# Kernel optimization log

Hardware: AMD Instinct MI355X
Metric: run time of the kernel (lower is better)

## Reference

```python
import jax, jax.numpy as jnp
import numpy as np

N, D, H, K = 131072, 512, 128, 3
NPOS, NNEG = 8192, 8192
KM_ITERS = 4
PROTO_SHIFT = 0.15
PROTO_LOGIT_SCALE = 0.2
TEMP = 2.5


def _sq_cdist(x, c):
    # squared euclidean distance, matches torch.cdist(...).pow(2)
    d = jnp.sum(x * x, -1, keepdims=True) + jnp.sum(c * c, -1)[None, :] - 2.0 * (x @ c.T)
    return jnp.maximum(d, 0.0)


def _kmeans(x, k, iters):
    # torch.linspace(0, n-1, steps=k).long() init, fixed iteration count
    n = x.shape[0]
    idx = jnp.linspace(0.0, n - 1, k).astype(jnp.int32)
    centers = x[idx]
    for _ in range(iters):
        assign = jnp.argmin(_sq_cdist(x, centers), axis=1)
        sums = jax.ops.segment_sum(x, assign, num_segments=k)
        counts = jax.ops.segment_sum(jnp.ones((n,), x.dtype), assign, num_segments=k)[:, None]
        # empty cluster keeps old center (mask.any() branch in torch)
        centers = jnp.where(counts > 0, sums / jnp.maximum(counts, 1.0), centers)
    return centers


def setup_inputs() -> dict:
    key = jax.random.key(0)
    ks = jax.random.split(key, 10)
    s = 1.0 / np.sqrt(D).astype(np.float32)
    return {
        "z_cls": jax.random.normal(ks[0], (N, D), jnp.float32),
        "z_proto": jax.random.normal(ks[1], (N, D), jnp.float32),
        "pos_ctx": jax.random.normal(ks[2], (D,), jnp.float32),
        "neg_ctx": jax.random.normal(ks[3], (D,), jnp.float32),
        "W1": jax.random.normal(ks[4], (H, D), jnp.float32) * s,
        "b1": jnp.zeros((H,), jnp.float32),
        "W2": jax.random.normal(ks[5], (1, H), jnp.float32) * (1.0 / np.sqrt(H).astype(np.float32)),
        "b2": jnp.zeros((1,), jnp.float32),
        "Wp": jax.random.normal(ks[6], (D, D), jnp.float32) * s,
        "bp": jnp.zeros((D,), jnp.float32),
        "Wn": jax.random.normal(ks[7], (D, D), jnp.float32) * s,
        "bn": jnp.zeros((D,), jnp.float32),
        "pos_idx": jax.random.randint(ks[8], (NPOS,), 0, N),
        "neg_idx": jax.random.randint(ks[9], (NNEG,), 0, N),
    }


def reference(z_cls, z_proto, pos_ctx, neg_ctx, W1, b1, W2, b2, Wp, bp, Wn, bn, pos_idx, neg_idx):
    # _build_prototypes (pos_idx/neg_idx nonempty path)
    pos_proto = _kmeans(z_proto[pos_idx], K, KM_ITERS)          # [K, D]
    neg_proto = jnp.mean(z_proto[neg_idx], axis=0)              # [D]
    # _calibrate (ema not initialized -> no EMA blend)
    pos_proto = pos_proto + PROTO_SHIFT * (pos_ctx @ Wp.T + bp)[None, :]
    neg_proto = neg_proto + PROTO_SHIFT * (neg_ctx @ Wn.T + bn)
    # distances
    d_pos_all = _sq_cdist(z_proto, pos_proto)                   # [N, K]
    d_pos = jnp.min(d_pos_all, axis=1)
    pos_assign = jnp.argmin(d_pos_all, axis=1)
    d_neg = jnp.mean((z_proto - neg_proto[None, :]) ** 2, axis=1)
    proto_logit = (d_neg - d_pos) / np.sqrt(D).astype(np.float32)
    # cls head (eval mode: dropout is identity)
    h = jax.nn.relu(z_cls @ W1.T + b1)
    cls_logit = (h @ W2.T + b2)[:, 0]
    logits = (cls_logit + PROTO_LOGIT_SCALE * proto_logit) / TEMP
    prob = jax.nn.sigmoid(logits)
    return (logits, prob, PROTO_LOGIT_SCALE * proto_logit, pos_assign, d_pos_all, pos_proto, neg_proto)
```

## Files before the change

### kernel.cpp

```cpp
#include <hip/hip_runtime.h>
#include <hip/hip_bf16.h>

#define NPTS 131072
#define DIM  512
#define HID  128
#define KCL  3
#define NPOSI 8192
#define NNEGI 8192

typedef __attribute__((ext_vector_type(8))) short bf16x8;
typedef __attribute__((ext_vector_type(4))) float f32x4;

#define ASG __attribute__((address_space(1)))
#define ASL __attribute__((address_space(3)))

enum {
  WS_SHIFT_POS = 0,
  WS_SHIFT_NEG = 512,
  WS_NEGSUM    = 1024,
  WS_NEGPART   = 1536,
  WS_SUMS      = 132608,
  WS_PPROTO    = 138764,
  WS_PN        = 140812,
  WS_W1FRAG    = 140816,
};
#define SUMS_STRIDE 1539

__device__ __forceinline__ short f2bf(float x) {
  __hip_bfloat16 h = __float2bfloat16(x);
  return *reinterpret_cast<short*>(&h);
}

__global__ __launch_bounds__(256, 1) void k_prep(const float* __restrict__ W1,
                                                 const float* __restrict__ Wp, const float* __restrict__ bp,
                                                 const float* __restrict__ Wn, const float* __restrict__ bn,
                                                 const float* __restrict__ pos_ctx, const float* __restrict__ neg_ctx,
                                                 const float* __restrict__ zp, const int* __restrict__ neg_idx,
                                                 float* __restrict__ ws) {
  int bid = blockIdx.x, t = threadIdx.x;
  if (bid < 32) {
    int fid = bid * 256 + t;
    int kc = fid >> 9;
    int n  = (fid >> 6) & 7;
    int l  = fid & 63;
    int row = n * 16 + (l & 15);
    int col = kc * 32 + (l >> 4) * 8;
    const float* src = W1 + (size_t)row * DIM + col;
    float4 v0 = *(const float4*)(src);
    float4 v1 = *(const float4*)(src + 4);
    bf16x8 f;
    f[0] = f2bf(v0.x); f[1] = f2bf(v0.y); f[2] = f2bf(v0.z); f[3] = f2bf(v0.w);
    f[4] = f2bf(v1.x); f[5] = f2bf(v1.y); f[6] = f2bf(v1.z); f[7] = f2bf(v1.w);
    ((bf16x8*)(ws + WS_W1FRAG))[fid] = f;
  } else if (bid < 64) {
    int b = bid - 32;
    int mat = b >> 4;
    const float* W    = mat ? Wn : Wp;
    const float* bias = mat ? bn : bp;
    const float* ctx  = mat ? neg_ctx : pos_ctx;
    float* outp = ws + (mat ? WS_SHIFT_NEG : WS_SHIFT_POS);
    int row = (b & 15) * 32 + (t >> 3);
    int sub = t & 7;
    const float* wr = W + row * DIM + sub * 64;
    const float* cr = ctx + sub * 64;
    float s = 0.f;
#pragma unroll
    for (int j = 0; j < 64; j += 4) {
      float4 w4 = *(const float4*)(wr + j);
      float4 c4 = *(const float4*)(cr + j);
      s += w4.x * c4.x + w4.y * c4.y + w4.z * c4.z + w4.w * c4.w;
    }
    s += __shfl_xor(s, 1);
    s += __shfl_xor(s, 2);
    s += __shfl_xor(s, 4);
    if (sub == 0) outp[row] = 0.15f * (s + bias[row]);
  } else if (bid < 320) {
    int jb = bid - 64;
    int c0 = t * 2;
    float a0 = 0.f, a1 = 0.f;
    int base = jb * 32;
#pragma unroll 8
    for (int jj = 0; jj < 32; ++jj) {
      int row = neg_idx[base + jj];
      float2 v = *(const float2*)(zp + (size_t)row * DIM + c0);
      a0 += v.x; a1 += v.y;
    }
    ws[WS_NEGPART + jb * DIM + c0]     = a0;
    ws[WS_NEGPART + jb * DIM + c0 + 1] = a1;
  } else {
    for (int idx = t; idx < 4 * SUMS_STRIDE; idx += 256) ws[WS_SUMS + idx] = 0.f;
  }
}

template <int IT>
__global__ __launch_bounds__(256) void k_km(const float* __restrict__ zp,
                                            const int* __restrict__ pos_idx,
                                            float* __restrict__ ws) {
  int bid = blockIdx.x, t = threadIdx.x;
  if (IT == 0 && bid == 256) {
    int c0 = t * 2;
    float a0 = 0.f, a1 = 0.f;
#pragma unroll 8
    for (int j = 0; j < 256; ++j) {
      float2 v = *(const float2*)(ws + WS_NEGPART + j * DIM + c0);
      a0 += v.x; a1 += v.y;
    }
    ws[WS_NEGSUM + c0]     = a0;
    ws[WS_NEGSUM + c0 + 1] = a1;
    return;
  }
  __shared__ float cc[KCL * DIM];
  __shared__ float cn[KCL];
  __shared__ float lsum[KCL * DIM];
  __shared__ float lcnt[KCL];
  int w = t >> 6, l = t & 63;

  for (int idx = t; idx < KCL * DIM; idx += 256) lsum[idx] = 0.f;
  if (t < KCL) lcnt[t] = 0.f;

  for (int idx = t; idx < KCL * DIM; idx += 256) {
    int k = idx >> 9;
    int sel = (k == 0) ? 0 : ((k == 1) ? 4095 : 8191);
    float v = zp[(size_t)pos_idx[sel] * DIM + (idx & 511)];
#pragma unroll
    for (int j = 0; j < IT; ++j) {
      float cntv = ws[WS_SUMS + j * SUMS_STRIDE + 3 * DIM + k];
      float sv   = ws[WS_SUMS + j * SUMS_STRIDE + idx];
      v = (cntv > 0.f) ? sv / cntv : v;
    }
    cc[idx] = v;
  }
  __syncthreads();
  if (w < KCL) {
    float s = 0.f;
#pragma unroll
    for (int m = 0; m < 8; ++m) { float v = cc[w * DIM + l + m * 64]; s += v * v; }
#pragma unroll
    for (int m = 1; m < 64; m <<= 1) s += __shfl_xor(s, m);
    if (l == 0) cn[w] = s;
  }
  __syncthreads();

  float ck0[8], ck1[8], ck2[8];
#pragma unroll
  for (int j = 0; j < 8; ++j) {
    ck0[j] = cc[0 * DIM + l * 8 + j];
    ck1[j] = cc[1 * DIM + l * 8 + j];
    ck2[j] = cc[2 * DIM + l * 8 + j];
  }
  float cn0 = cn[0], cn1 = cn[1], cn2 = cn[2];
  float acc0[8] = {0,0,0,0,0,0,0,0}, acc1[8] = {0,0,0,0,0,0,0,0}, acc2[8] = {0,0,0,0,0,0,0,0};
  float cnt0 = 0.f, cnt1 = 0.f, cnt2 = 0.f;

  int wid = bid * 4 + w;
#pragma unroll 2
  for (int p = wid; p < NPOSI; p += 1024) {
    int row = pos_idx[p];
    const float* xr = zp + (size_t)row * DIM + l * 8;
    float4 x0 = *(const float4*)(xr);
    float4 x1 = *(const float4*)(xr + 4);
    float x[8] = {x0.x, x0.y, x0.z, x0.w, x1.x, x1.y, x1.z, x1.w};
    float d0 = 0.f, d1 = 0.f, d2 = 0.f;
#pragma unroll
    for (int j = 0; j < 8; ++j) { d0 += x[j] * ck0[j]; d1 += x[j] * ck1[j]; d2 += x[j] * ck2[j]; }
#pragma unroll
    for (int m = 1; m < 64; m <<= 1) {
      d0 += __shfl_xor(d0, m); d1 += __shfl_xor(d1, m); d2 += __shfl_xor(d2, m);
    }
    float t0 = cn0 - 2.f * d0, t1 = cn1 - 2.f * d1, t2 = cn2 - 2.f * d2;
    int a = 0; float best = t0;
    if (t1 < best) { best = t1; a = 1; }
    if (t2 < best) { best = t2; a = 2; }
    if (a == 0)      { cnt0 += 1.f;
#pragma unroll
      for (int j = 0; j < 8; ++j) acc0[j] += x[j]; }
    else if (a == 1) { cnt1 += 1.f;
#pragma unroll
      for (int j = 0; j < 8; ++j) acc1[j] += x[j]; }
    else             { cnt2 += 1.f;
#pragma unroll
      for (int j = 0; j < 8; ++j) acc2[j] += x[j]; }
  }
#pragma unroll
  for (int j = 0; j < 8; ++j) {
    atomicAdd(&lsum[0 * DIM + l * 8 + j], acc0[j]);
    atomicAdd(&lsum[1 * DIM + l * 8 + j], acc1[j]);
    atomicAdd(&lsum[2 * DIM + l * 8 + j], acc2[j]);
  }
  if (l == 0) {
    atomicAdd(&lcnt[0], cnt0); atomicAdd(&lcnt[1], cnt1); atomicAdd(&lcnt[2], cnt2);
  }
  __syncthreads();
  for (int idx = t; idx < KCL * DIM; idx += 256) atomicAdd(&ws[WS_SUMS + IT * SUMS_STRIDE + idx], lsum[idx]);
  if (t < KCL) atomicAdd(&ws[WS_SUMS + IT * SUMS_STRIDE + 3 * DIM + t], lcnt[t]);
}

__global__ __launch_bounds__(256) void k_fin(const float* __restrict__ zp,
                                             const int* __restrict__ pos_idx,
                                             float* __restrict__ ws, float* __restrict__ out) {
  __shared__ __align__(16) float pp[4 * DIM];
  int t = threadIdx.x, w = t >> 6, l = t & 63;
  for (int idx = t; idx < KCL * DIM; idx += 256) {
    int k = idx >> 9, d = idx & 511;
    int sel = (k == 0) ? 0 : ((k == 1) ? 4095 : 8191);
    float v = zp[(size_t)pos_idx[sel] * DIM + d];
#pragma unroll
    for (int j = 0; j < 4; ++j) {
      float cntv = ws[WS_SUMS + j * SUMS_STRIDE + 3 * DIM + k];
      float sv   = ws[WS_SUMS + j * SUMS_STRIDE + idx];
      v = (cntv > 0.f) ? sv / cntv : v;
    }
    pp[idx] = v + ws[WS_SHIFT_POS + d];
  }
  for (int d = t; d < DIM; d += 256)
    pp[3 * DIM + d] = ws[WS_NEGSUM + d] * (1.f / NNEGI) + ws[WS_SHIFT_NEG + d];
  __syncthreads();
  {
    float s = 0.f;
#pragma unroll
    for (int m = 0; m < 8; ++m) { float v = pp[w * DIM + l + m * 64]; s += v * v; }
#pragma unroll
    for (int m = 1; m < 64; m <<= 1) s += __shfl_xor(s, m);
    if (l == 0) ws[WS_PN + w] = s;
  }
  for (int idx = t; idx < 4 * DIM; idx += 256) {
    ws[WS_PPROTO + idx] = pp[idx];
    out[7 * NPTS + idx] = pp[idx];
  }
}

__global__ __launch_bounds__(512) void k_fused(const float* __restrict__ zc,
                                               const float* __restrict__ zp,
                                               const float* __restrict__ b1,
                                               const float* __restrict__ W2,
                                               const float* __restrict__ b2,
                                               const float* __restrict__ ws,
                                               float* __restrict__ out) {
  __shared__ __align__(16) float Azc[16 * DIM];
  __shared__ __align__(16) float Azp[16 * DIM];
  __shared__ __align__(16) float pp[4 * DIM];
  __shared__ float pns[4];
  __shared__ float clsv[16];

  int t = threadIdx.x, w = t >> 6, l = t & 63;
  int bid = (blockIdx.x & 7) * 1024 + (blockIdx.x >> 3);
  int i0 = bid * 16;

  {
    int cg = (w < 4);
    int r0 = (cg ? w : (w - 4)) * 4;
    const float* gsrc = (cg ? zc : zp) + (size_t)(i0 + r0) * DIM;
    float* ldsb = cg ? Azc : Azp;
#pragma unroll
    for (int r = 0; r < 4; ++r) {
      int rloc = r0 + r;
      int swz = (rloc & 7) << 2;
#pragma unroll
      for (int seg = 0; seg < 2; ++seg) {
        int c = seg * 256 + ((l * 4) ^ swz);
        __builtin_amdgcn_global_load_lds((const ASG void*)(gsrc + (size_t)r * DIM + c),
                                         (ASL void*)&ldsb[rloc * DIM + seg * 256], 16, 0, 0);
      }
    }
  }

  if (t < 512) ((float4*)pp)[t] = ((const float4*)(ws + WS_PPROTO))[t];
  if (t < 16) clsv[t] = 0.f;
  if (t < 4) pns[t] = ws[WS_PN + t];
  int col_l = l & 15;
  float b1c[2], w2c[2], b2v = b2[0];
  if (w < 4) {
#pragma unroll
    for (int nn = 0; nn < 2; ++nn) {
      int col = (w * 2 + nn) * 16 + col_l;
      b1c[nn] = b1[col];
      w2c[nn] = W2[col];
    }
  }
  __syncthreads();

  float rd0 = 0.f, rd1 = 0.f, rd2 = 0.f, rdn = 0.f, rsx = 0.f;
  if (w < 4) {
    const bf16x8* w1f = (const bf16x8*)(ws + WS_W1FRAG);
    int sub = l >> 4, arow = l & 15;
    int swz = (arow & 7) << 2;
    int abase = arow * DIM;
    f32x4 acc[2];
    acc[0] = (f32x4){0.f, 0.f, 0.f, 0.f};
    acc[1] = (f32x4){0.f, 0.f, 0.f, 0.f};
    bf16x8 B2[3][2];
#pragma unroll
    for (int pf = 0; pf < 3; ++pf)
#pragma unroll
      for (int nn = 0; nn < 2; ++nn)
        B2[pf][nn] = w1f[pf * 512 + (w * 2 + nn) * 64 + l];

#pragma unroll
    for (int kc = 0; kc < 16; ++kc) {
      int g = kc * 32 + sub * 8;
      float4 a0 = *(const float4*)&Azc[abase + (g ^ swz)];
      float4 a1 = *(const float4*)&Azc[abase + ((g + 4) ^ swz)];
      if (kc + 3 < 16) {
#pragma unroll
        for (int nn = 0; nn < 2; ++nn)
          B2[kc % 3][nn] = w1f[(kc + 3) * 512 + (w * 2 + nn) * 64 + l];
      }
      bf16x8 af;
      af[0] = f2bf(a0.x); af[1] = f2bf(a0.y); af[2] = f2bf(a0.z); af[3] = f2bf(a0.w);
      af[4] = f2bf(a1.x); af[5] = f2bf(a1.y); af[6] = f2bf(a1.z); af[7] = f2bf(a1.w);
#pragma unroll
      for (int nn = 0; nn < 2; ++nn)
        acc[nn] = __builtin_amdgcn_mfma_f32_16x16x32_bf16(af, B2[kc % 3][nn], acc[nn], 0, 0, 0);
    }
    float prt[4] = {0.f, 0.f, 0.f, 0.f};
#pragma unroll
    for (int nn = 0; nn < 2; ++nn) {
#pragma unroll
      for (int r = 0; r < 4; ++r) {
        float h = acc[nn][r] + b1c[nn];
        h = h > 0.f ? h : 0.f;
        prt[r] += h * w2c[nn];
      }
    }
#pragma unroll
    for (int m = 1; m < 16; m <<= 1) {
#pragma unroll
      for (int r = 0; r < 4; ++r) prt[r] += __shfl_xor(prt[r], m);
    }
    if (col_l == 0) {
      float add = (w == 0) ? b2v : 0.f;
#pragma unroll
      for (int r = 0; r < 4; ++r)
        atomicAdd(&clsv[sub * 4 + r], prt[r] + add);
    }
  } else {
    int s = l & 15, r4 = l >> 4;
    int rloc = (w - 4) * 4 + r4;
    int swz = (rloc & 7) << 2;
    int xbase = rloc * DIM;
#pragma unroll
    for (int j = 0; j < 8; ++j) {
      int c = j * 64 + s * 4;
      float4 x  = *(const float4*)&Azp[xbase + (c ^ swz)];
      float4 c0 = *(const float4*)&pp[0 * DIM + c];
      float4 c1 = *(const float4*)&pp[1 * DIM + c];
      float4 c2 = *(const float4*)&pp[2 * DIM + c];
      float4 c3 = *(const float4*)&pp[3 * DIM + c];
      rd0 += x.x * c0.x + x.y * c0.y + x.z * c0.z + x.w * c0.w;
      rd1 += x.x * c1.x + x.y * c1.y + x.z * c1.z + x.w * c1.w;
      rd2 += x.x * c2.x + x.y * c2.y + x.z * c2.z + x.w * c2.w;
      rdn += x.x * c3.x + x.y * c3.y + x.z * c3.z + x.w * c3.w;
      rsx += x.x * x.x  + x.y * x.y  + x.z * x.z  + x.w * x.w;
    }
#pragma unroll
    for (int m = 1; m < 16; m <<= 1) {
      rd0 += __shfl_xor(rd0, m);
      rd1 += __shfl_xor(rd1, m);
      rd2 += __shfl_xor(rd2, m);
      rdn += __shfl_xor(rdn, m);
      rsx += __shfl_xor(rsx, m);
    }
  }
  __syncthreads();

  if (w >= 4 && (l & 15) == 0) {
    int rloc = (w - 4) * 4 + (l >> 4);
    int i = i0 + rloc;
    float e0 = rsx + pns[0] - 2.f * rd0; e0 = fmaxf(e0, 0.f);
    float e1 = rsx + pns[1] - 2.f * rd1; e1 = fmaxf(e1, 0.f);
    float e2 = rsx + pns[2] - 2.f * rd2; e2 = fmaxf(e2, 0.f);
    float dpos = e0; int a = 0;
    if (e1 < dpos) { dpos = e1; a = 1; }
    if (e2 < dpos) { dpos = e2; a = 2; }
    float dneg = (rsx + pns[3] - 2.f * rdn) * (1.f / DIM);
    float plog = (dneg - dpos) * 0.04419417382415922f;
    float o2 = 0.2f * plog;
    float lg = (clsv[rloc] + o2) * 0.4f;
    float prob = 1.f / (1.f + expf(-lg));
    out[i]            = lg;
    out[NPTS + i]     = prob;
    out[2 * NPTS + i] = o2;
    out[3 * NPTS + i] = (float)a;
    out[4 * NPTS + 3 * i]     = e0;
    out[4 * NPTS + 3 * i + 1] = e1;
    out[4 * NPTS + 3 * i + 2] = e2;
  }
}

extern "C" void kernel_launch(void* const* d_in, const int* in_sizes, int n_in,
                              void* d_out, int out_size, void* d_ws, size_t ws_size,
                              hipStream_t stream) {
  const float* z_cls   = (const float*)d_in[0];
  const float* z_proto = (const float*)d_in[1];
  const float* pos_ctx = (const float*)d_in[2];
  const float* neg_ctx = (const float*)d_in[3];
  const float* W1      = (const float*)d_in[4];
  const float* b1      = (const float*)d_in[5];
  const float* W2      = (const float*)d_in[6];
  const float* b2      = (const float*)d_in[7];
  const float* Wp      = (const float*)d_in[8];
  const float* bp      = (const float*)d_in[9];
  const float* Wn      = (const float*)d_in[10];
  const float* bn      = (const float*)d_in[11];
  const int* pos_idx   = (const int*)d_in[12];
  const int* neg_idx   = (const int*)d_in[13];
  float* out           = (float*)d_out;
  float* ws            = (float*)d_ws;

  k_prep<<<321, 256, 0, stream>>>(W1, Wp, bp, Wn, bn, pos_ctx, neg_ctx, z_proto, neg_idx, ws);
  k_km<0><<<257, 256, 0, stream>>>(z_proto, pos_idx, ws);
  k_km<1><<<256, 256, 0, stream>>>(z_proto, pos_idx, ws);
  k_km<2><<<256, 256, 0, stream>>>(z_proto, pos_idx, ws);
  k_km<3><<<256, 256, 0, stream>>>(z_proto, pos_idx, ws);
  k_fin<<<1, 256, 0, stream>>>(z_proto, pos_idx, ws, out);
  k_fused<<<NPTS / 16, 512, 0, stream>>>(z_cls, z_proto, b1, W2, b2, ws, out);
}
```

Baseline: 283.8 us.

## Split fused kernel into separate cls-head and prototype-distance kernels

Splits the single fused kernel into k_cls, which computes the MLP head logits from z_cls into workspace and launches before the k-means kernels, and k_proto, which computes the prototype distances from z_proto and reads back the cls logits. The aim is better occupancy, with smaller LDS footprints and explicit launch bounds, and simpler per-kernel schedules. The cost is an extra launch and a workspace round trip for the cls logits. Since everything stays on one stream, k_cls does not actually overlap with k-means.

Measured after the change: 261.2 us. 1.09x faster.

```diff
diff --git a/kernel.cpp b/kernel.cpp
--- a/kernel.cpp
+++ b/kernel.cpp
@@ -23,6 +23,7 @@
   WS_PPROTO    = 138764,
   WS_PN        = 140812,
   WS_W1FRAG    = 140816,
+  WS_CLSL      = 173584,
 };
 #define SUMS_STRIDE 1539
 
@@ -229,17 +230,12 @@
   }
 }
 
-__global__ __launch_bounds__(512) void k_fused(const float* __restrict__ zc,
-                                               const float* __restrict__ zp,
-                                               const float* __restrict__ b1,
-                                               const float* __restrict__ W2,
-                                               const float* __restrict__ b2,
-                                               const float* __restrict__ ws,
-                                               float* __restrict__ out) {
+__global__ __launch_bounds__(256, 4) void k_cls(const float* __restrict__ zc,
+                                                const float* __restrict__ b1,
+                                                const float* __restrict__ W2,
+                                                const float* __restrict__ b2,
+                                                float* __restrict__ ws) {
   __shared__ __align__(16) float Azc[16 * DIM];
-  __shared__ __align__(16) float Azp[16 * DIM];
-  __shared__ __align__(16) float pp[4 * DIM];
-  __shared__ float pns[4];
   __shared__ float clsv[16];
 
   int t = threadIdx.x, w = t >> 6, l = t & 63;
@@ -247,40 +243,32 @@
   int i0 = bid * 16;
 
   {
-    int cg = (w < 4);
-    int r0 = (cg ? w : (w - 4)) * 4;
-    const float* gsrc = (cg ? zc : zp) + (size_t)(i0 + r0) * DIM;
-    float* ldsb = cg ? Azc : Azp;
+    const float* gsrc = zc + (size_t)(i0 + w * 4) * DIM;
 #pragma unroll
     for (int r = 0; r < 4; ++r) {
-      int rloc = r0 + r;
+      int rloc = w * 4 + r;
       int swz = (rloc & 7) << 2;
 #pragma unroll
       for (int seg = 0; seg < 2; ++seg) {
         int c = seg * 256 + ((l * 4) ^ swz);
         __builtin_amdgcn_global_load_lds((const ASG void*)(gsrc + (size_t)r * DIM + c),
-                                         (ASL void*)&ldsb[rloc * DIM + seg * 256], 16, 0, 0);
+                                         (ASL void*)&Azc[rloc * DIM + seg * 256], 16, 0, 0);
       }
     }
   }
-
-  if (t < 512) ((float4*)pp)[t] = ((const float4*)(ws + WS_PPROTO))[t];
   if (t < 16) clsv[t] = 0.f;
-  if (t < 4) pns[t] = ws[WS_PN + t];
   int col_l = l & 15;
-  float b1c[2], w2c[2], b2v = b2[0];
-  if (w < 4) {
-#pragma unroll
-    for (int nn = 0; nn < 2; ++nn) {
-      int col = (w * 2 + nn) * 16 + col_l;
-      b1c[nn] = b1[col];
-      w2c[nn] = W2[col];
-    }
-  }
-  __syncthreads();
-
-  float rd0 = 0.f, rd1 = 0.f, rd2 = 0.f, rdn = 0.f, rsx = 0.f;
-  if (w < 4) {
+  float b1c[2], w2c[2];
+#pragma unroll
+  for (int nn = 0; nn < 2; ++nn) {
+    int col = (w * 2 + nn) * 16 + col_l;
+    b1c[nn] = b1[col];
+    w2c[nn] = W2[col];
+  }
+  float b2v = b2[0];
+  __syncthreads();
+
+  {
     const bf16x8* w1f = (const bf16x8*)(ws + WS_W1FRAG);
     int sub = l >> 4, arow = l & 15;
     int swz = (arow & 7) << 2;
@@ -333,49 +321,80 @@
       for (int r = 0; r < 4; ++r)
         atomicAdd(&clsv[sub * 4 + r], prt[r] + add);
     }
-  } else {
-    int s = l & 15, r4 = l >> 4;
-    int rloc = (w - 4) * 4 + r4;
-    int swz = (rloc & 7) << 2;
-    int xbase = rloc * DIM;
-#pragma unroll
-    for (int j = 0; j < 8; ++j) {
-      int c = j * 64 + s * 4;
-      float4 x  = *(const float4*)&Azp[xbase + (c ^ swz)];
-      float4 c0 = *(const float4*)&pp[0 * DIM + c];
-      float4 c1 = *(const float4*)&pp[1 * DIM + c];
-      float4 c2 = *(const float4*)&pp[2 * DIM + c];
-      float4 c3 = *(const float4*)&pp[3 * DIM + c];
-      rd0 += x.x * c0.x + x.y * c0.y + x.z * c0.z + x.w * c0.w;
-      rd1 += x.x * c1.x + x.y * c1.y + x.z * c1.z + x.w * c1.w;
-      rd2 += x.x * c2.x + x.y * c2.y + x.z * c2.z + x.w * c2.w;
-      rdn += x.x * c3.x + x.y * c3.y + x.z * c3.z + x.w * c3.w;
-      rsx += x.x * x.x  + x.y * x.y  + x.z * x.z  + x.w * x.w;
-    }
-#pragma unroll
-    for (int m = 1; m < 16; m <<= 1) {
-      rd0 += __shfl_xor(rd0, m);
-      rd1 += __shfl_xor(rd1, m);
-      rd2 += __shfl_xor(rd2, m);
-      rdn += __shfl_xor(rdn, m);
-      rsx += __shfl_xor(rsx, m);
-    }
-  }
-  __syncthreads();
-
-  if (w >= 4 && (l & 15) == 0) {
-    int rloc = (w - 4) * 4 + (l >> 4);
+  }
+  __syncthreads();
+  if (t < 16) ws[WS_CLSL + i0 + t] = clsv[t];
+}
+
+__global__ __launch_bounds__(256, 3) void k_proto(const float* __restrict__ zp,
+                                                  const float* __restrict__ ws,
+                                                  float* __restrict__ out) {
+  __shared__ __align__(16) float Azp[16 * DIM];
+  __shared__ __align__(16) float pp[4 * DIM];
+  __shared__ float pns[4];
+
+  int t = threadIdx.x, w = t >> 6, l = t & 63;
+  int bid = (blockIdx.x & 7) * 1024 + (blockIdx.x >> 3);
+  int i0 = bid * 16;
+
+  {
+    const float* gsrc = zp + (size_t)(i0 + w * 4) * DIM;
+#pragma unroll
+    for (int r = 0; r < 4; ++r) {
+      int rloc = w * 4 + r;
+      int swz = (rloc & 7) << 2;
+#pragma unroll
+      for (int seg = 0; seg < 2; ++seg) {
+        int c = seg * 256 + ((l * 4) ^ swz);
+        __builtin_amdgcn_global_load_lds((const ASG void*)(gsrc + (size_t)r * DIM + c),
+                                         (ASL void*)&Azp[rloc * DIM + seg * 256], 16, 0, 0);
+      }
+    }
+  }
+  for (int idx = t; idx < 512; idx += 256)
+    ((float4*)pp)[idx] = ((const float4*)(ws + WS_PPROTO))[idx];
+  if (t < 4) pns[t] = ws[WS_PN + t];
+  __syncthreads();
+
+  int s = l & 15, r4 = l >> 4;
+  int rloc = w * 4 + r4;
+  int swz = (rloc & 7) << 2;
+  int xbase = rloc * DIM;
+  float d0 = 0.f, d1 = 0.f, d2 = 0.f, dn = 0.f, sx = 0.f;
+#pragma unroll
+  for (int j = 0; j < 8; ++j) {
+    int c = j * 64 + s * 4;
+    float4 x  = *(const float4*)&Azp[xbase + (c ^ swz)];
+    float4 c0 = *(const float4*)&pp[0 * DIM + c];
+    float4 c1 = *(const float4*)&pp[1 * DIM + c];
+    float4 c2 = *(const float4*)&pp[2 * DIM + c];
+    float4 c3 = *(const float4*)&pp[3 * DIM + c];
+    d0 += x.x * c0.x + x.y * c0.y + x.z * c0.z + x.w * c0.w;
+    d1 += x.x * c1.x + x.y * c1.y + x.z * c1.z + x.w * c1.w;
+    d2 += x.x * c2.x + x.y * c2.y + x.z * c2.z + x.w * c2.w;
+    dn += x.x * c3.x + x.y * c3.y + x.z * c3.z + x.w * c3.w;
+    sx += x.x * x.x  + x.y * x.y  + x.z * x.z  + x.w * x.w;
+  }
+#pragma unroll
+  for (int m = 1; m < 16; m <<= 1) {
+    d0 += __shfl_xor(d0, m);
+    d1 += __shfl_xor(d1, m);
+    d2 += __shfl_xor(d2, m);
+    dn += __shfl_xor(dn, m);
+    sx += __shfl_xor(sx, m);
+  }
+  if (s == 0) {
     int i = i0 + rloc;
-    float e0 = rsx + pns[0] - 2.f * rd0; e0 = fmaxf(e0, 0.f);
-    float e1 = rsx + pns[1] - 2.f * rd1; e1 = fmaxf(e1, 0.f);
-    float e2 = rsx + pns[2] - 2.f * rd2; e2 = fmaxf(e2, 0.f);
+    float e0 = sx + pns[0] - 2.f * d0; e0 = fmaxf(e0, 0.f);
+    float e1 = sx + pns[1] - 2.f * d1; e1 = fmaxf(e1, 0.f);
+    float e2 = sx + pns[2] - 2.f * d2; e2 = fmaxf(e2, 0.f);
     float dpos = e0; int a = 0;
     if (e1 < dpos) { dpos = e1; a = 1; }
     if (e2 < dpos) { dpos = e2; a = 2; }
-    float dneg = (rsx + pns[3] - 2.f * rdn) * (1.f / DIM);
+    float dneg = (sx + pns[3] - 2.f * dn) * (1.f / DIM);
     float plog = (dneg - dpos) * 0.04419417382415922f;
     float o2 = 0.2f * plog;
-    float lg = (clsv[rloc] + o2) * 0.4f;
+    float lg = (ws[WS_CLSL + i] + o2) * 0.4f;
     float prob = 1.f / (1.f + expf(-lg));
     out[i]            = lg;
     out[NPTS + i]     = prob;
@@ -408,10 +427,11 @@
   float* ws            = (float*)d_ws;
 
   k_prep<<<321, 256, 0, stream>>>(W1, Wp, bp, Wn, bn, pos_ctx, neg_ctx, z_proto, neg_idx, ws);
+  k_cls<<<NPTS / 16, 256, 0, stream>>>(z_cls, b1, W2, b2, ws);
   k_km<0><<<257, 256, 0, stream>>>(z_proto, pos_idx, ws);
   k_km<1><<<256, 256, 0, stream>>>(z_proto, pos_idx, ws);
   k_km<2><<<256, 256, 0, stream>>>(z_proto, pos_idx, ws);
   k_km<3><<<256, 256, 0, stream>>>(z_proto, pos_idx, ws);
   k_fin<<<1, 256, 0, stream>>>(z_proto, pos_idx, ws, out);
-  k_fused<<<NPTS / 16, 512, 0, stream>>>(z_cls, z_proto, b1, W2, b2, ws, out);
-}
+  k_proto<<<NPTS / 16, 256, 0, stream>>>(z_proto, ws, out);
+}
```
